# Performance work log

Measured on AMD Instinct MI355X. Metric: run time of the kernel, lower is better.

## Reference

```python
import jax, jax.numpy as jnp
import numpy as np

D_MODEL = 1024
NUM_HEADS = 16
D_K = D_MODEL // NUM_HEADS
B, S = 4, 2048


def setup_inputs() -> dict:
    key = jax.random.key(0)
    ks = jax.random.split(key, 12)
    scale = 1.0 / np.sqrt(D_MODEL)
    inp = {
        "Q": jax.random.normal(ks[0], (B, S, D_MODEL), dtype=jnp.float32),
        "K": jax.random.normal(ks[1], (B, S, D_MODEL), dtype=jnp.float32),
        "V": jax.random.normal(ks[2], (B, S, D_MODEL), dtype=jnp.float32),
        # causal mask broadcast over batch and heads; masked_fill where mask==0
        "mask": jnp.tril(jnp.ones((S, S), dtype=jnp.int32))[None, None, :, :],
        "Wq": jax.random.normal(ks[3], (D_MODEL, D_MODEL), dtype=jnp.float32) * scale,
        "bq": jnp.zeros((D_MODEL,), dtype=jnp.float32),
        "Wk": jax.random.normal(ks[4], (D_MODEL, D_MODEL), dtype=jnp.float32) * scale,
        "bk": jnp.zeros((D_MODEL,), dtype=jnp.float32),
        "Wv": jax.random.normal(ks[5], (D_MODEL, D_MODEL), dtype=jnp.float32) * scale,
        "bv": jnp.zeros((D_MODEL,), dtype=jnp.float32),
        "Wo": jax.random.normal(ks[6], (D_MODEL, D_MODEL), dtype=jnp.float32) * scale,
        "bo": jnp.zeros((D_MODEL,), dtype=jnp.float32),
    }
    return inp


def _split_heads(x):
    b, s, _ = x.shape
    return x.reshape(b, s, NUM_HEADS, D_K).transpose(0, 2, 1, 3)  # [B,H,S,Dk]


def reference(Q, K, V, mask, Wq, bq, Wk, bk, Wv, bv, Wo, bo):
    # torch nn.Linear: x @ W.T + b
    q = _split_heads(Q @ Wq.T + bq)
    k = _split_heads(K @ Wk.T + bk)
    v = _split_heads(V @ Wv.T + bv)
    scores = jnp.einsum("bhsd,bhtd->bhst", q, k) / jnp.sqrt(jnp.float32(D_K))
    scores = jnp.where(mask == 0, jnp.float32(-1e9), scores)
    probs = jax.nn.softmax(scores, axis=-1)  # dropout is identity in eval mode
    ctx = jnp.einsum("bhst,bhtd->bhsd", probs, v)
    ctx = ctx.transpose(0, 2, 1, 3).reshape(Q.shape[0], Q.shape[1], D_MODEL)
    out = ctx @ Wo.T + bo
    return out, probs
```

## Files before the change

kernel.cpp:

```cpp
#include <hip/hip_runtime.h>
#include <stdint.h>

typedef unsigned short u16;
typedef unsigned int u32;
typedef __attribute__((ext_vector_type(2))) unsigned int u32x2;
typedef __attribute__((ext_vector_type(8))) short short8;
typedef __attribute__((ext_vector_type(4))) float f32x4;
typedef __attribute__((ext_vector_type(4))) unsigned int u32x4;

#define SEQ 2048
#define DM 1024
#define NH 16
#define NBH 64
#define MR 8192

#define GLOAD16(g, l) __builtin_amdgcn_global_load_lds( \
    (const __attribute__((address_space(1))) void*)(g), \
    (__attribute__((address_space(3))) void*)(l), 16, 0, 0)

#define VMCNT(N) asm volatile("s_waitcnt vmcnt(" #N ")" ::: "memory")

__device__ __forceinline__ u16 f2bf(float f) {
  u32 u = __float_as_uint(f);
  u32 r = u + 0x7fffu + ((u >> 16) & 1u);
  return (u16)(r >> 16);
}
__device__ __forceinline__ u32 cvtpk_bf16(float lo, float hi) {
  u32 r;
  asm("v_cvt_pk_bf16_f32 %0, %1, %2" : "=v"(r) : "v"(lo), "v"(hi));
  return r;
}

__global__ __launch_bounds__(256) void cvt_all(
    const float* __restrict__ Q, const float* __restrict__ K, const float* __restrict__ V,
    const float* __restrict__ Wq, const float* __restrict__ Wk, const float* __restrict__ Wv,
    const float* __restrict__ Wo,
    u16* __restrict__ dQ, u16* __restrict__ dK, u16* __restrict__ dV,
    u16* __restrict__ dWq, u16* __restrict__ dWk, u16* __restrict__ dWv, u16* __restrict__ dWo) {
  int b = blockIdx.x;
  const float* s; u16* d; size_t off;
  if (b < 4096)       { s = Q;  d = dQ;  off = (size_t)b * 2048; }
  else if (b < 8192)  { s = K;  d = dK;  off = (size_t)(b - 4096) * 2048; }
  else if (b < 12288) { s = V;  d = dV;  off = (size_t)(b - 8192) * 2048; }
  else if (b < 12800) { s = Wq; d = dWq; off = (size_t)(b - 12288) * 2048; }
  else if (b < 13312) { s = Wk; d = dWk; off = (size_t)(b - 12800) * 2048; }
  else if (b < 13824) { s = Wv; d = dWv; off = (size_t)(b - 13312) * 2048; }
  else                { s = Wo; d = dWo; off = (size_t)(b - 13824) * 2048; }
  size_t i = off + (size_t)threadIdx.x * 8;
  float4 x = *(const float4*)(s + i);
  float4 y = *(const float4*)(s + i + 4);
  u32x4 o;
  o.x = (u32)f2bf(x.x) | ((u32)f2bf(x.y) << 16);
  o.y = (u32)f2bf(x.z) | ((u32)f2bf(x.w) << 16);
  o.z = (u32)f2bf(y.x) | ((u32)f2bf(y.y) << 16);
  o.w = (u32)f2bf(y.z) | ((u32)f2bf(y.w) << 16);
  *(u32x4*)(d + i) = o;
}

__device__ __forceinline__ void gemm_body(
    const u16* __restrict__ A, const u16* __restrict__ Bw, const float* __restrict__ bias,
    void* __restrict__ Cp, int wg, int MODE) {
  const int bn = wg & 7;
  const int bm = wg >> 3;
  __shared__ u16 As[2][128 * 64];
  __shared__ u16 Bs[2][128 * 64];
  const int tid = threadIdx.x;
  const int lane = tid & 63, wave = tid >> 6;
  const int wr = wave >> 1, wc = wave & 1;
  const int g16 = lane >> 4, l16 = lane & 15;
  f32x4 acc[4][4] = {};

  const int srow = lane >> 3;
  const int sblk = (lane & 7) ^ srow;
  const u16* Abase = A + (size_t)(bm * 128) * DM + sblk * 8;
  const u16* Bbase = Bw + (size_t)(bn * 128) * DM + sblk * 8;

  auto stage = [&](int kt) {
#pragma unroll
    for (int i = 0; i < 4; ++i) {
      const int r0 = wave * 32 + i * 8;
      GLOAD16(Abase + (size_t)(r0 + srow) * DM + kt * 64, (char*)As[kt & 1] + r0 * 128);
      GLOAD16(Bbase + (size_t)(r0 + srow) * DM + kt * 64, (char*)Bs[kt & 1] + r0 * 128);
    }
  };

  stage(0);
  for (int kt = 0; kt < 16; ++kt) {
    VMCNT(0);
    __builtin_amdgcn_s_barrier();
    if (kt + 1 < 16) stage(kt + 1);
    const char* Ab = (const char*)As[kt & 1];
    const char* Bb = (const char*)Bs[kt & 1];
#pragma unroll
    for (int ks = 0; ks < 2; ++ks) {
      short8 af[4], bfr[4];
#pragma unroll
      for (int m = 0; m < 4; ++m) {
        const int r = wr * 64 + m * 16 + l16;
        af[m] = *(const short8*)(Ab + ((r * 128 + ks * 64 + g16 * 16) ^ ((r & 7) << 4)));
      }
#pragma unroll
      for (int n = 0; n < 4; ++n) {
        const int r = wc * 64 + n * 16 + l16;
        bfr[n] = *(const short8*)(Bb + ((r * 128 + ks * 64 + g16 * 16) ^ ((r & 7) << 4)));
      }
#pragma unroll
      for (int m = 0; m < 4; ++m)
#pragma unroll
        for (int n = 0; n < 4; ++n)
          acc[m][n] = __builtin_amdgcn_mfma_f32_16x16x32_bf16(af[m], bfr[n], acc[m][n], 0, 0, 0);
    }
  }
#pragma unroll
  for (int m = 0; m < 4; ++m)
#pragma unroll
    for (int n = 0; n < 4; ++n) {
      int col = bn * 128 + wc * 64 + n * 16 + l16;
      float bs = bias[col];
      if (MODE == 2) {
        int row0 = bm * 128 + wr * 64 + m * 16 + g16 * 4;
        int bb = row0 >> 11, ss = row0 & 2047;
        int hh = col >> 6, dd = col & 63;
        u32 lo = (u32)f2bf(acc[m][n][0] + bs) | ((u32)f2bf(acc[m][n][1] + bs) << 16);
        u32 hi = (u32)f2bf(acc[m][n][2] + bs) | ((u32)f2bf(acc[m][n][3] + bs) << 16);
        *(u32x2*)((u16*)Cp + (((size_t)(bb * NH + hh) * 64 + dd) * SEQ + ss)) = (u32x2){lo, hi};
      } else {
#pragma unroll
        for (int r = 0; r < 4; ++r) {
          int row = bm * 128 + wr * 64 + m * 16 + g16 * 4 + r;
          float v = acc[m][n][r] + bs;
          if (MODE == 0) {
            int bb = row >> 11, ss = row & 2047, hh = col >> 6, dd = col & 63;
            ((u16*)Cp)[((((size_t)bb * NH + hh) * SEQ + ss) << 6) + dd] = f2bf(v);
          } else {
            ((float*)Cp)[(size_t)row * DM + col] = v;
          }
        }
      }
    }
}

__global__ __launch_bounds__(256) void gemm_qkv(
    const u16* __restrict__ Qb, const u16* __restrict__ Wqb, const float* __restrict__ bq, u16* __restrict__ qhp,
    const u16* __restrict__ Kb, const u16* __restrict__ Wkb, const float* __restrict__ bk, u16* __restrict__ khp,
    const u16* __restrict__ Vb, const u16* __restrict__ Wvb, const float* __restrict__ bv, u16* __restrict__ vtp) {
  const int bid = blockIdx.x;
  const int sel = bid >> 9;
  const int inner = bid & 511;
  const int wg = (inner & 7) * 64 + (inner >> 3);
  if (sel == 0)      gemm_body(Qb, Wqb, bq, qhp, wg, 0);
  else if (sel == 1) gemm_body(Kb, Wkb, bk, khp, wg, 0);
  else               gemm_body(Vb, Wvb, bv, vtp, wg, 2);
}

__global__ __launch_bounds__(256) void gemm_out(
    const u16* __restrict__ A, const u16* __restrict__ Bw, const float* __restrict__ bias,
    float* __restrict__ Cp) {
  const int bid = blockIdx.x;
  const int wg = (bid & 7) * 64 + (bid >> 3);
  gemm_body(A, Bw, bias, Cp, wg, 1);
}

__global__ __launch_bounds__(512, 4) void attn_fwd(
    const u16* __restrict__ qh, const u16* __restrict__ kh, const u16* __restrict__ vt,
    float* __restrict__ probs, u16* __restrict__ ctx) {
  const int bid = blockIdx.x;
  const int wg = (bid & 7) * 128 + (bid >> 3);
  const int qt = 15 - (wg & 15);
  const int bh = wg >> 4;
  const int tid = threadIdx.x;
  const int lane = tid & 63, wave = tid >> 6;
  const int g16 = lane >> 4, l16 = lane & 15;
  __shared__ __align__(16) char SLDS[81920];
  char* Ps = SLDS + 65536;

  const int qglob = qt * 128 + wave * 16 + l16;
  short8 qf0, qf1;
  {
    const u16* qp = qh + ((size_t)bh * SEQ + qglob) * 64 + g16 * 8;
    qf0 = *(const short8*)qp;
    qf1 = *(const short8*)(qp + 32);
  }
  float lrow = 0.f;
  const float SL2 = 0.125f * 1.44269504088896f;

  const int srow = wave * 8 + (lane >> 3);
  const int sblk = (lane & 7) ^ (lane >> 3);
  const u16* kS = kh + ((size_t)bh * SEQ + srow) * 64 + sblk * 8;
  const int vrow0 = wave * 8 + (lane >> 4);
  const u16* vS0 = vt + ((size_t)bh * 64 + vrow0) * SEQ + (((lane & 15) ^ (vrow0 & 7)) * 8);
  const int vrow1 = vrow0 + 4;
  const u16* vS1 = vt + ((size_t)bh * 64 + vrow1) * SEQ + (((lane & 15) ^ (vrow1 & 7)) * 8);

  auto qk64 = [&](const char* Kb, int ss, f32x4 (&sc)[4]) {
#pragma unroll
    for (int ks = 0; ks < 2; ++ks) {
      const short8 qf = ks ? qf1 : qf0;
#pragma unroll
      for (int f = 0; f < 4; ++f) {
        const int t = ss * 64 + f * 16 + l16;
        const short8 kb = *(const short8*)(Kb + ((t * 128 + ks * 64 + g16 * 16) ^ ((t & 7) << 4)));
        sc[f] = __builtin_amdgcn_mfma_f32_16x16x32_bf16(kb, qf, sc[f], 0, 0, 0);
      }
    }
  };

  const int ntokA = (qt + 1) * 128;
  const int n256 = (qt + 2) >> 1;
  auto stageA = [&](int kt) {
#pragma unroll
    for (int i = 0; i < 4; ++i)
      GLOAD16(kS + ((size_t)kt * 256 + i * 64) * 64,
              SLDS + (kt & 1) * 32768 + i * 8192 + wave * 1024);
  };
  stageA(0);
  for (int kt = 0; kt < n256; ++kt) {
    VMCNT(0);
    __builtin_amdgcn_s_barrier();
    if (kt + 1 < n256) stageA(kt + 1);
    const char* Kb = SLDS + (kt & 1) * 32768;
    float s = 0.f;
#pragma unroll
    for (int ss = 0; ss < 4; ++ss) {
      const int t0 = kt * 256 + ss * 64;
      if (t0 >= ntokA) break;
      f32x4 sc[4] = {};
      __builtin_amdgcn_s_setprio(1);
      qk64(Kb, ss, sc);
      __builtin_amdgcn_s_setprio(0);
      const bool fullt = (t0 + 63 <= qt * 128 + wave * 16);
      if (fullt) {
#pragma unroll
        for (int f = 0; f < 4; ++f)
#pragma unroll
          for (int r = 0; r < 4; ++r)
            s += exp2f(sc[f][r] * SL2);
      } else {
#pragma unroll
        for (int f = 0; f < 4; ++f)
#pragma unroll
          for (int r = 0; r < 4; ++r) {
            const int k = t0 + f * 16 + g16 * 4 + r;
            s += (k <= qglob) ? exp2f(sc[f][r] * SL2) : 0.f;
          }
      }
    }
    s += __shfl_xor(s, 16);
    s += __shfl_xor(s, 32);
    lrow += s;
  }
  const float rinv = 1.f / lrow;

  f32x4 acc[4] = {};
  const size_t prowB = ((size_t)bh * SEQ + qglob) * SEQ;
  const int prow = wave * 16 + l16;
  const int nkB = qt + 1;

  __syncthreads();
  auto stageBK = [&](int kt) {
#pragma unroll
    for (int i = 0; i < 2; ++i)
      GLOAD16(kS + ((size_t)kt * 128 + i * 64) * 64,
              SLDS + (kt & 1) * 16384 + i * 8192 + wave * 1024);
  };
  auto stageBV = [&](int kt) {
    GLOAD16(vS0 + kt * 128, SLDS + 32768 + (kt & 1) * 16384 + wave * 2048);
    GLOAD16(vS1 + kt * 128, SLDS + 32768 + (kt & 1) * 16384 + wave * 2048 + 1024);
  };
  stageBK(0); stageBV(0);
  for (int kt = 0; kt < nkB; ++kt) {
    if (kt == 0) VMCNT(0); else VMCNT(8);
    __builtin_amdgcn_s_barrier();
    if (kt + 1 < nkB) { stageBK(kt + 1); stageBV(kt + 1); }
    const char* Kb = SLDS + (kt & 1) * 16384;
    const char* Vb = SLDS + 32768 + (kt & 1) * 16384;
#pragma unroll
    for (int ss = 0; ss < 2; ++ss) {
      f32x4 sc[4] = {};
      __builtin_amdgcn_s_setprio(1);
      qk64(Kb, ss, sc);
      __builtin_amdgcn_s_setprio(0);
      const int t0 = kt * 128 + ss * 64;
      const bool fullt = (t0 + 63 <= qt * 128 + wave * 16);
#pragma unroll
      for (int f = 0; f < 4; ++f) {
        float pv[4];
        if (fullt) {
#pragma unroll
          for (int r = 0; r < 4; ++r) pv[r] = exp2f(sc[f][r] * SL2) * rinv;
        } else {
#pragma unroll
          for (int r = 0; r < 4; ++r) {
            const int k = t0 + f * 16 + g16 * 4 + r;
            pv[r] = (k <= qglob) ? exp2f(sc[f][r] * SL2) * rinv : 0.f;
          }
        }
        *(f32x4*)(probs + prowB + t0 + f * 16 + g16 * 4) =
            (f32x4){pv[0], pv[1], pv[2], pv[3]};
        u32x2 pk = {cvtpk_bf16(pv[0], pv[1]), cvtpk_bf16(pv[2], pv[3])};
        *(u32x2*)(Ps + ((prow * 128 + f * 32 + g16 * 8) ^ ((prow & 7) << 4))) = pk;
      }
      __builtin_amdgcn_s_setprio(1);
#pragma unroll
      for (int ks = 0; ks < 2; ++ks) {
        const short8 pa = *(const short8*)(Ps + ((prow * 128 + ks * 64 + g16 * 16) ^ ((prow & 7) << 4)));
#pragma unroll
        for (int cf = 0; cf < 4; ++cf) {
          const int dd = cf * 16 + l16;
          const short8 vb = *(const short8*)(Vb + ((dd * 256 + ss * 128 + ks * 64 + g16 * 16) ^ ((dd & 7) << 4)));
          acc[cf] = __builtin_amdgcn_mfma_f32_16x16x32_bf16(pa, vb, acc[cf], 0, 0, 0);
        }
      }
      __builtin_amdgcn_s_setprio(0);
    }
  }

  {
    const size_t zrow = ((size_t)bh * SEQ + qt * 128 + wave * 16 + (lane >> 2)) * SEQ;
    const int pcol = (lane & 3) * 16;
    const f32x4 z = {0.f, 0.f, 0.f, 0.f};
    for (int c0 = nkB * 128 + pcol; c0 < SEQ; c0 += 64) {
      float* dst = probs + zrow + c0;
      *(f32x4*)(dst) = z;
      *(f32x4*)(dst + 4) = z;
      *(f32x4*)(dst + 8) = z;
      *(f32x4*)(dst + 12) = z;
    }
  }

#pragma unroll
  for (int cf = 0; cf < 4; ++cf)
#pragma unroll
    for (int r = 0; r < 4; ++r) {
      const int srw = qt * 128 + wave * 16 + g16 * 4 + r;
      const size_t o = ((size_t)(bh >> 4) * SEQ + srw) * DM + (bh & 15) * 64 + cf * 16 + l16;
      ctx[o] = f2bf(acc[cf][r]);
    }
}

extern "C" void kernel_launch(void* const* d_in, const int* in_sizes, int n_in,
                              void* d_out, int out_size, void* d_ws, size_t ws_size,
                              hipStream_t stream) {
  (void)in_sizes; (void)n_in; (void)out_size; (void)ws_size;
  const float* Q  = (const float*)d_in[0];
  const float* K  = (const float*)d_in[1];
  const float* V  = (const float*)d_in[2];
  const float* Wq = (const float*)d_in[4];
  const float* bq = (const float*)d_in[5];
  const float* Wk = (const float*)d_in[6];
  const float* bk = (const float*)d_in[7];
  const float* Wv = (const float*)d_in[8];
  const float* bv = (const float*)d_in[9];
  const float* Wo = (const float*)d_in[10];
  const float* bo = (const float*)d_in[11];

  char* ws = (char*)d_ws;
  const size_t MB = 1024 * 1024;
  u16* Qb  = (u16*)(ws + 0 * MB);
  u16* Kb  = (u16*)(ws + 16 * MB);
  u16* Vb  = (u16*)(ws + 32 * MB);
  u16* Wqb = (u16*)(ws + 48 * MB);
  u16* Wkb = (u16*)(ws + 50 * MB);
  u16* Wvb = (u16*)(ws + 52 * MB);
  u16* Wob = (u16*)(ws + 54 * MB);
  u16* qhp = (u16*)(ws + 56 * MB);
  u16* khp = (u16*)(ws + 72 * MB);
  u16* vtp = (u16*)(ws + 88 * MB);
  u16* ctx = Kb;

  float* outp = (float*)d_out;
  float* probs = outp + (size_t)MR * DM;

  cvt_all<<<14336, 256, 0, stream>>>(Q, K, V, Wq, Wk, Wv, Wo, Qb, Kb, Vb, Wqb, Wkb, Wvb, Wob);
  gemm_qkv<<<1536, 256, 0, stream>>>(Qb, Wqb, bq, qhp, Kb, Wkb, bk, khp, Vb, Wvb, bv, vtp);
  attn_fwd<<<1024, 512, 0, stream>>>(qhp, khp, vtp, probs, ctx);
  gemm_out<<<512, 256, 0, stream>>>(ctx, Wob, bo, outp);
}
```

Before: 425.5 us.

## Double attention query tile per block to reuse K/V tiles across 256 rows

Measured after the change: 671.3 us. 57.8% more time.

```diff
diff --git a/kernel.cpp b/kernel.cpp
--- a/kernel.cpp
+++ b/kernel.cpp
@@ -162,26 +162,27 @@
 }
 
 __global__ __launch_bounds__(512, 4) void attn_fwd(
-    const u16* __restrict__ qh, const u16* __restrict__ kh, const u16* __restrict__ vt,
+    const u16* __restrict__ qh_, const u16* __restrict__ kh, const u16* __restrict__ vt,
     float* __restrict__ probs, u16* __restrict__ ctx) {
   const int bid = blockIdx.x;
-  const int wg = (bid & 7) * 128 + (bid >> 3);
-  const int qt = 15 - (wg & 15);
-  const int bh = wg >> 4;
+  const int xcd = bid & 7;
+  const int j = bid >> 3;
+  const int bh = xcd * 8 + (j & 7);
+  const int qt = (j < 32) ? (7 - (j >> 3)) : ((j - 32) >> 3);
   const int tid = threadIdx.x;
   const int lane = tid & 63, wave = tid >> 6;
   const int g16 = lane >> 4, l16 = lane & 15;
   __shared__ __align__(16) char SLDS[81920];
   char* Ps = SLDS + 65536;
 
-  const int qglob = qt * 128 + wave * 16 + l16;
-  short8 qf0, qf1;
-  {
-    const u16* qp = qh + ((size_t)bh * SEQ + qglob) * 64 + g16 * 8;
-    qf0 = *(const short8*)qp;
-    qf1 = *(const short8*)(qp + 32);
-  }
-  float lrow = 0.f;
+  const int wq = qt * 256 + wave * 32;
+  short8 qf[2][2];
+#pragma unroll
+  for (int h = 0; h < 2; ++h) {
+    const u16* qp = qh_ + ((size_t)bh * SEQ + wq + h * 16 + l16) * 64 + g16 * 8;
+    qf[h][0] = *(const short8*)qp;
+    qf[h][1] = *(const short8*)(qp + 32);
+  }
   const float SL2 = 0.125f * 1.44269504088896f;
 
   const int srow = wave * 8 + (lane >> 3);
@@ -192,69 +193,74 @@
   const int vrow1 = vrow0 + 4;
   const u16* vS1 = vt + ((size_t)bh * 64 + vrow1) * SEQ + (((lane & 15) ^ (vrow1 & 7)) * 8);
 
-  auto qk64 = [&](const char* Kb, int ss, f32x4 (&sc)[4]) {
-#pragma unroll
-    for (int ks = 0; ks < 2; ++ks) {
-      const short8 qf = ks ? qf1 : qf0;
-#pragma unroll
-      for (int f = 0; f < 4; ++f) {
-        const int t = ss * 64 + f * 16 + l16;
-        const short8 kb = *(const short8*)(Kb + ((t * 128 + ks * 64 + g16 * 16) ^ ((t & 7) << 4)));
-        sc[f] = __builtin_amdgcn_mfma_f32_16x16x32_bf16(kb, qf, sc[f], 0, 0, 0);
-      }
-    }
-  };
-
-  const int ntokA = (qt + 1) * 128;
-  const int n256 = (qt + 2) >> 1;
+  const int nkA = qt + 1;
   auto stageA = [&](int kt) {
 #pragma unroll
     for (int i = 0; i < 4; ++i)
       GLOAD16(kS + ((size_t)kt * 256 + i * 64) * 64,
               SLDS + (kt & 1) * 32768 + i * 8192 + wave * 1024);
   };
+  float lacc[2] = {0.f, 0.f};
   stageA(0);
-  for (int kt = 0; kt < n256; ++kt) {
+  for (int kt = 0; kt < nkA; ++kt) {
     VMCNT(0);
     __builtin_amdgcn_s_barrier();
-    if (kt + 1 < n256) stageA(kt + 1);
+    if (kt + 1 < nkA) stageA(kt + 1);
     const char* Kb = SLDS + (kt & 1) * 32768;
-    float s = 0.f;
 #pragma unroll
     for (int ss = 0; ss < 4; ++ss) {
       const int t0 = kt * 256 + ss * 64;
-      if (t0 >= ntokA) break;
-      f32x4 sc[4] = {};
+      if (t0 > wq + 31) break;
+      f32x4 sc[2][4] = {};
       __builtin_amdgcn_s_setprio(1);
-      qk64(Kb, ss, sc);
+#pragma unroll
+      for (int ks = 0; ks < 2; ++ks)
+#pragma unroll
+        for (int f = 0; f < 4; ++f) {
+          const int t = ss * 64 + f * 16 + l16;
+          const short8 kb = *(const short8*)(Kb + ((t * 128 + ks * 64 + g16 * 16) ^ ((t & 7) << 4)));
+          sc[0][f] = __builtin_amdgcn_mfma_f32_16x16x32_bf16(kb, qf[0][ks], sc[0][f], 0, 0, 0);
+          sc[1][f] = __builtin_amdgcn_mfma_f32_16x16x32_bf16(kb, qf[1][ks], sc[1][f], 0, 0, 0);
+        }
       __builtin_amdgcn_s_setprio(0);
-      const bool fullt = (t0 + 63 <= qt * 128 + wave * 16);
-      if (fullt) {
-#pragma unroll
-        for (int f = 0; f < 4; ++f)
-#pragma unroll
-          for (int r = 0; r < 4; ++r)
-            s += exp2f(sc[f][r] * SL2);
-      } else {
-#pragma unroll
-        for (int f = 0; f < 4; ++f)
-#pragma unroll
-          for (int r = 0; r < 4; ++r) {
-            const int k = t0 + f * 16 + g16 * 4 + r;
-            s += (k <= qglob) ? exp2f(sc[f][r] * SL2) : 0.f;
-          }
-      }
-    }
+#pragma unroll
+      for (int h = 0; h < 2; ++h) {
+        if (t0 > wq + h * 16 + 15) continue;
+        if (t0 + 63 <= wq + h * 16) {
+#pragma unroll
+          for (int f = 0; f < 4; ++f)
+#pragma unroll
+            for (int r = 0; r < 4; ++r)
+              lacc[h] += exp2f(sc[h][f][r] * SL2);
+        } else {
+          const int qg = wq + h * 16 + l16;
+#pragma unroll
+          for (int f = 0; f < 4; ++f)
+#pragma unroll
+            for (int r = 0; r < 4; ++r) {
+              const int k = t0 + f * 16 + g16 * 4 + r;
+              lacc[h] += (k <= qg) ? exp2f(sc[h][f][r] * SL2) : 0.f;
+            }
+        }
+      }
+    }
+  }
+  float rinv[2];
+#pragma unroll
+  for (int h = 0; h < 2; ++h) {
+    float s = lacc[h];
     s += __shfl_xor(s, 16);
     s += __shfl_xor(s, 32);
-    lrow += s;
-  }
-  const float rinv = 1.f / lrow;
-
-  f32x4 acc[4] = {};
-  const size_t prowB = ((size_t)bh * SEQ + qglob) * SEQ;
+    rinv[h] = 1.f / s;
+  }
+
+  f32x4 acc[2][4] = {};
+  size_t prowB[2];
+#pragma unroll
+  for (int h = 0; h < 2; ++h)
+    prowB[h] = ((size_t)bh * SEQ + wq + h * 16 + l16) * SEQ;
   const int prow = wave * 16 + l16;
-  const int nkB = qt + 1;
+  const int nkB = 2 * qt + 2;
 
   __syncthreads();
   auto stageBK = [&](int kt) {
@@ -269,73 +275,105 @@
   };
   stageBK(0); stageBV(0);
   for (int kt = 0; kt < nkB; ++kt) {
-    if (kt == 0) VMCNT(0); else VMCNT(8);
+    if (kt == 0) VMCNT(0); else VMCNT(16);
     __builtin_amdgcn_s_barrier();
     if (kt + 1 < nkB) { stageBK(kt + 1); stageBV(kt + 1); }
     const char* Kb = SLDS + (kt & 1) * 16384;
     const char* Vb = SLDS + 32768 + (kt & 1) * 16384;
 #pragma unroll
     for (int ss = 0; ss < 2; ++ss) {
-      f32x4 sc[4] = {};
+      const int t0 = kt * 128 + ss * 64;
+      const f32x4 z4 = {0.f, 0.f, 0.f, 0.f};
+      if (t0 > wq + 31) {
+#pragma unroll
+        for (int h = 0; h < 2; ++h)
+#pragma unroll
+          for (int f = 0; f < 4; ++f)
+            *(f32x4*)(probs + prowB[h] + t0 + f * 16 + g16 * 4) = z4;
+        continue;
+      }
+      f32x4 sc[2][4] = {};
       __builtin_amdgcn_s_setprio(1);
-      qk64(Kb, ss, sc);
+#pragma unroll
+      for (int ks = 0; ks < 2; ++ks)
+#pragma unroll
+        for (int f = 0; f < 4; ++f) {
+          const int t = ss * 64 + f * 16 + l16;
+          const short8 kb = *(const short8*)(Kb + ((t * 128 + ks * 64 + g16 * 16) ^ ((t & 7) << 4)));
+          sc[0][f] = __builtin_amdgcn_mfma_f32_16x16x32_bf16(kb, qf[0][ks], sc[0][f], 0, 0, 0);
+          sc[1][f] = __builtin_amdgcn_mfma_f32_16x16x32_bf16(kb, qf[1][ks], sc[1][f], 0, 0, 0);
+        }
       __builtin_amdgcn_s_setprio(0);
-      const int t0 = kt * 128 + ss * 64;
-      const bool fullt = (t0 + 63 <= qt * 128 + wave * 16);
-#pragma unroll
-      for (int f = 0; f < 4; ++f) {
-        float pv[4];
-        if (fullt) {
-#pragma unroll
-          for (int r = 0; r < 4; ++r) pv[r] = exp2f(sc[f][r] * SL2) * rinv;
-        } else {
-#pragma unroll
-          for (int r = 0; r < 4; ++r) {
-            const int k = t0 + f * 16 + g16 * 4 + r;
-            pv[r] = (k <= qglob) ? exp2f(sc[f][r] * SL2) * rinv : 0.f;
+#pragma unroll
+      for (int h = 0; h < 2; ++h) {
+        if (t0 > wq + h * 16 + 15) {
+#pragma unroll
+          for (int f = 0; f < 4; ++f)
+            *(f32x4*)(probs + prowB[h] + t0 + f * 16 + g16 * 4) = z4;
+          continue;
+        }
+        const bool fullt = (t0 + 63 <= wq + h * 16);
+#pragma unroll
+        for (int f = 0; f < 4; ++f) {
+          float pv[4];
+          if (fullt) {
+#pragma unroll
+            for (int r = 0; r < 4; ++r) pv[r] = exp2f(sc[h][f][r] * SL2) * rinv[h];
+          } else {
+            const int qg = wq + h * 16 + l16;
+#pragma unroll
+            for (int r = 0; r < 4; ++r) {
+              const int k = t0 + f * 16 + g16 * 4 + r;
+              pv[r] = (k <= qg) ? exp2f(sc[h][f][r] * SL2) * rinv[h] : 0.f;
+            }
           }
-        }
-        *(f32x4*)(probs + prowB + t0 + f * 16 + g16 * 4) =
-            (f32x4){pv[0], pv[1], pv[2], pv[3]};
-        u32x2 pk = {cvtpk_bf16(pv[0], pv[1]), cvtpk_bf16(pv[2], pv[3])};
-        *(u32x2*)(Ps + ((prow * 128 + f * 32 + g16 * 8) ^ ((prow & 7) << 4))) = pk;
-      }
-      __builtin_amdgcn_s_setprio(1);
-#pragma unroll
-      for (int ks = 0; ks < 2; ++ks) {
-        const short8 pa = *(const short8*)(Ps + ((prow * 128 + ks * 64 + g16 * 16) ^ ((prow & 7) << 4)));
-#pragma unroll
-        for (int cf = 0; cf < 4; ++cf) {
-          const int dd = cf * 16 + l16;
-          const short8 vb = *(const short8*)(Vb + ((dd * 256 + ss * 128 + ks * 64 + g16 * 16) ^ ((dd & 7) << 4)));
-          acc[cf] = __builtin_amdgcn_mfma_f32_16x16x32_bf16(pa, vb, acc[cf], 0, 0, 0);
-        }
-      }
-      __builtin_amdgcn_s_setprio(0);
+          *(f32x4*)(probs + prowB[h] + t0 + f * 16 + g16 * 4) =
+              (f32x4){pv[0], pv[1], pv[2], pv[3]};
+          u32x2 pk = {cvtpk_bf16(pv[0], pv[1]), cvtpk_bf16(pv[2], pv[3])};
+          *(u32x2*)(Ps + ((prow * 128 + f * 32 + g16 * 8) ^ ((prow & 7) << 4))) = pk;
+        }
+        __builtin_amdgcn_s_setprio(1);
+#pragma unroll
+        for (int ks = 0; ks < 2; ++ks) {
+          const short8 pa = *(const short8*)(Ps + ((prow * 128 + ks * 64 + g16 * 16) ^ ((prow & 7) << 4)));
+#pragma unroll
+          for (int cf = 0; cf < 4; ++cf) {
+            const int dd = cf * 16 + l16;
+            const short8 vb = *(const short8*)(Vb + ((dd * 256 + ss * 128 + ks * 64 + g16 * 16) ^ ((dd & 7) << 4)));
+            acc[h][cf] = __builtin_amdgcn_mfma_f32_16x16x32_bf16(pa, vb, acc[h][cf], 0, 0, 0);
+          }
+        }
+        __builtin_amdgcn_s_setprio(0);
+      }
     }
   }
 
   {
-    const size_t zrow = ((size_t)bh * SEQ + qt * 128 + wave * 16 + (lane >> 2)) * SEQ;
     const int pcol = (lane & 3) * 16;
     const f32x4 z = {0.f, 0.f, 0.f, 0.f};
-    for (int c0 = nkB * 128 + pcol; c0 < SEQ; c0 += 64) {
-      float* dst = probs + zrow + c0;
-      *(f32x4*)(dst) = z;
-      *(f32x4*)(dst + 4) = z;
-      *(f32x4*)(dst + 8) = z;
-      *(f32x4*)(dst + 12) = z;
-    }
-  }
-
-#pragma unroll
-  for (int cf = 0; cf < 4; ++cf)
-#pragma unroll
-    for (int r = 0; r < 4; ++r) {
-      const int srw = qt * 128 + wave * 16 + g16 * 4 + r;
-      const size_t o = ((size_t)(bh >> 4) * SEQ + srw) * DM + (bh & 15) * 64 + cf * 16 + l16;
-      ctx[o] = f2bf(acc[cf][r]);
-    }
+#pragma unroll
+    for (int h = 0; h < 2; ++h) {
+      const size_t zrow = ((size_t)bh * SEQ + qt * 256 + wave * 32 + h * 16 + (lane >> 2)) * SEQ;
+      for (int c0 = nkB * 128 + pcol; c0 < SEQ; c0 += 64) {
+        float* dst = probs + zrow + c0;
+        *(f32x4*)(dst) = z;
+        *(f32x4*)(dst + 4) = z;
+        *(f32x4*)(dst + 8) = z;
+        *(f32x4*)(dst + 12) = z;
+      }
+    }
+  }
+
+#pragma unroll
+  for (int h = 0; h < 2; ++h)
+#pragma unroll
+    for (int cf = 0; cf < 4; ++cf)
+#pragma unroll
+      for (int r = 0; r < 4; ++r) {
+        const int srw = qt * 256 + wave * 32 + h * 16 + g16 * 4 + r;
+        const size_t o = ((size_t)(bh >> 4) * SEQ + srw) * DM + (bh & 15) * 64 + cf * 16 + l16;
+        ctx[o] = f2bf(acc[h][cf][r]);
+      }
 }
 
 extern "C" void kernel_launch(void* const* d_in, const int* in_sizes, int n_in,
@@ -373,6 +411,6 @@
 
   cvt_all<<<14336, 256, 0, stream>>>(Q, K, V, Wq, Wk, Wv, Wo, Qb, Kb, Vb, Wqb, Wkb, Wvb, Wob);
   gemm_qkv<<<1536, 256, 0, stream>>>(Qb, Wqb, bq, qhp, Kb, Wkb, bk, khp, Vb, Wvb, bv, vtp);
-  attn_fwd<<<1024, 512, 0, stream>>>(qhp, khp, vtp, probs, ctx);
+  attn_fwd<<<512, 512, 0, stream>>>(qhp, khp, vtp, probs, ctx);
   gemm_out<<<512, 256, 0, stream>>>(ctx, Wob, bo, outp);
 }
```
